# Optimization experiments

Measured on AMD Instinct MI355X. Metric: run time of the kernel, lower is better.

Reference implementation:

```python
import jax, jax.numpy as jnp
import numpy as np

ATOM_VOC = 128
APO = 128
NHEAD = 16
D_MODEL = 512
BOND_VOC = 32
CHIRAL_VOC = 4
B, L = 4, 384


def setup_inputs() -> dict:
    key = jax.random.key(0)
    ks = jax.random.split(key, 12)
    atoms = jax.random.randint(ks[0], (B, L), 0, ATOM_VOC)
    chirals = jax.random.randint(ks[1], (B, L), 0, CHIRAL_VOC)
    coordinates = jax.random.normal(ks[2], (B, L, 3), dtype=jnp.float32)
    bonds = jax.random.randint(ks[3], (B, L, L), 0, BOND_VOC)
    # embedding tables; padding_idx rows (0) zeroed to match torch padding_idx
    atype_emb = jax.random.normal(ks[4], (ATOM_VOC, D_MODEL), dtype=jnp.float32) * 0.02
    atype_emb = atype_emb.at[0].set(0.0)
    chiral_emb = jax.random.normal(ks[5], (CHIRAL_VOC, D_MODEL), dtype=jnp.float32) * 0.02
    chiral_emb = chiral_emb.at[0].set(0.0)
    apair_w_emb = jax.random.normal(ks[6], (ATOM_VOC * ATOM_VOC, APO), dtype=jnp.float32) * 0.02
    apair_b_emb = jax.random.normal(ks[7], (ATOM_VOC * ATOM_VOC, APO), dtype=jnp.float32) * 0.02
    means = jax.random.normal(ks[8], (APO,), dtype=jnp.float32) * 0.1
    stds = jnp.ones((APO,), dtype=jnp.float32) + jax.random.normal(ks[9], (APO,), dtype=jnp.float32) * 0.1
    bond_emb = jax.random.normal(ks[10], (BOND_VOC, NHEAD), dtype=jnp.float32) * 0.02
    bond_emb = bond_emb.at[0].set(0.0)
    lin_w = jax.random.normal(ks[11], (NHEAD, APO), dtype=jnp.float32) * (1.0 / np.sqrt(APO))
    lin_b = jnp.zeros((NHEAD,), dtype=jnp.float32)
    return dict(atoms=atoms, chirals=chirals, coordinates=coordinates, bonds=bonds,
                atype_emb=atype_emb, chiral_emb=chiral_emb,
                apair_w_emb=apair_w_emb, apair_b_emb=apair_b_emb,
                means=means, stds=stds, bond_emb=bond_emb, lin_w=lin_w, lin_b=lin_b)


def reference(atoms, chirals, coordinates, bonds, atype_emb, chiral_emb,
              apair_w_emb, apair_b_emb, means, stds, bond_emb, lin_w, lin_b):
    # atoms: [b,l] int; coordinates: [b,l,3]; bonds: [b,l,l] int
    atoms_emb = atype_emb[atoms] + chiral_emb[chirals]          # [b,l,d]
    atoms_emb = jnp.transpose(atoms_emb, (1, 0, 2))             # [l,b,d]
    diff = coordinates[:, None, :, :] - coordinates[:, :, None, :]  # [b,l,l,3]
    d2 = jnp.sum(diff * diff, axis=-1)
    distances = jnp.sqrt(d2 + 1e-12)                            # [b,l,l] (eps avoids nan grad on diag)
    apair_idx = atoms[:, None, :] * ATOM_VOC + atoms[:, :, None]  # [b,l,l]
    ap = apair_w_emb[apair_idx] * distances[..., None] + apair_b_emb[apair_idx]  # [b,l,l,apo]
    s = jnp.abs(stds) + 1e-5
    ap = jnp.exp(-0.5 * jnp.square((ap - means) / s)) / (np.sqrt(2 * np.pi) * s)
    ap = jnp.einsum('bijk,hk->bijh', ap, lin_w) + lin_b + bond_emb[bonds]  # [b,l,l,nhead]
    pad = (atoms == 0)[:, None, :, None]                        # mask key atoms (dim 2)
    ap = jnp.where(pad, -jnp.inf, ap)
    ap = jnp.transpose(ap, (0, 3, 1, 2))                        # [b,nhead,l,l]
    return atoms_emb, ap
```

## Files before the change

kernel.cpp:

```cpp
#include <hip/hip_runtime.h>
#include <hip/hip_fp16.h>
#include <math.h>
#include <string.h>

#define ATOM_VOC 128
#define APO      128
#define NHEAD    16
#define D_MODEL  512
#define NB       4
#define NL       384

typedef __attribute__((ext_vector_type(8))) _Float16 f16x8;
typedef __attribute__((ext_vector_type(4))) float    f32x4;
typedef __attribute__((ext_vector_type(4))) unsigned u32x4;

#define PACK_DWORDS (ATOM_VOC * ATOM_VOC * APO)
#define BFT_SHORTS  (4 * 4 * 16 * 8)

static __device__ inline unsigned short f2h(float x) {
    __half h = __float2half(x);
    unsigned short u; memcpy(&u, &h, 2); return u;
}

__global__ __launch_bounds__(128) void pack_kernel(
    const float* __restrict__ apw, const float* __restrict__ apb,
    const float* __restrict__ means, const float* __restrict__ stds,
    const float* __restrict__ lin_w,
    unsigned* __restrict__ pack, unsigned short* __restrict__ bft, int write_bft)
{
    const int t    = threadIdx.x;
    const int v    = blockIdx.x;
    const int ai   = blockIdx.y;
    const int half = t >> 6;
    const int p    = t & 63;
    const int k0   = 2 * p, k1 = 2 * p + 1;

    const float s0  = fabsf(stds[k0]) + 1e-5f;
    const float s1  = fabsf(stds[k1]) + 1e-5f;
    const float ag0 = 0.84932180028802f / s0;
    const float ag1 = 0.84932180028802f / s1;

    const size_t srcrow = ((size_t)v * ATOM_VOC + ai) * APO;
    float x0, x1;
    if (half == 0) {
        x0 = apw[srcrow + k0] * ag0;
        x1 = apw[srcrow + k1] * ag1;
    } else {
        x0 = (apb[srcrow + k0] - means[k0]) * ag0;
        x1 = (apb[srcrow + k1] - means[k1]) * ag1;
    }
    pack[((size_t)ai * ATOM_VOC + v) * APO + half * 64 + p] =
        ((unsigned)f2h(x1) << 16) | f2h(x0);

    if (write_bft && v == 0 && ai == 0) {
#pragma unroll
        for (int hh = 0; hh < 2; ++hh) {
            const int cid  = t + hh * 128;
            const int ks   = cid >> 6;
            const int quad = (cid >> 4) & 3;
            const int h    = cid & 15;
            const int kb   = ks * 32 + quad * 8;
            unsigned short tmp[8];
#pragma unroll
            for (int u = 0; u < 8; ++u) {
                const int kk = kb + u;
                float z = 0.3989422804014327f / (fabsf(stds[kk]) + 1e-5f);
                tmp[u] = f2h(lin_w[h * APO + kk] * z);
            }
            memcpy(&bft[(size_t)cid * 8], tmp, 16);
        }
    }
}

__global__ __launch_bounds__(256) void atoms_emb_kernel(
    const int* __restrict__ atoms, const int* __restrict__ chirals,
    const float* __restrict__ atype_emb, const float* __restrict__ chiral_emb,
    float* __restrict__ out)
{
    const int D4 = D_MODEL / 4;
    int t = blockIdx.x * 256 + threadIdx.x;
    if (t >= NL * NB * D4) return;
    int d4 = t % D4;
    int bl = t / D4;
    int b  = bl % NB;
    int l  = bl / NB;
    int a  = atoms[b * NL + l];
    int c  = chirals[b * NL + l];
    float4 va = ((const float4*)(atype_emb  + (size_t)a * D_MODEL))[d4];
    float4 vc = ((const float4*)(chiral_emb + (size_t)c * D_MODEL))[d4];
    float4 o;
    o.x = va.x + vc.x; o.y = va.y + vc.y; o.z = va.z + vc.z; o.w = va.w + vc.w;
    ((float4*)out)[t] = o;
}

__global__ __launch_bounds__(512, 4) void ap_kernel(
    const int*            __restrict__ atoms,
    const float*          __restrict__ coords,
    const int*            __restrict__ bonds,
    const unsigned*       __restrict__ pack,
    const unsigned short* __restrict__ bft,
    const float*          __restrict__ bond_emb,
    const float*          __restrict__ lin_b,
    float*                __restrict__ out)
{
    const int i    = blockIdx.x;
    const int b    = blockIdx.y;
    const int t    = threadIdx.x;
    const int lane = t & 63;
    const int wave = t >> 6;
    const int h    = lane & 15;
    const int quad = lane >> 4;

    __shared__ unsigned tbl[ATOM_VOC * APO];

    const int ai = atoms[b * NL + i];

    const unsigned* src = pack + (size_t)ai * (ATOM_VOC * APO);
#pragma unroll
    for (int it = 0; it < 8; ++it) {
        int c    = it * 512 + t;
        int v    = c >> 5;
        int cc   = c & 31;
        int hlf  = cc >> 4;
        int cp   = cc & 15;
        u32x4 d  = ((const u32x4*)src)[c];
        *(u32x4*)&tbl[v * APO + hlf * 64 + 4 * (cp ^ (v & 15))] = d;
    }

    f16x8 bfrag[4];
#pragma unroll
    for (int ks = 0; ks < 4; ++ks)
        memcpy(&bfrag[ks], bft + ((size_t)((ks * 4 + quad) * 16 + h)) * 8, 16);
    const float lbh = lin_b[h];

    const float cix = coords[((size_t)b * NL + i) * 3 + 0];
    const float ciy = coords[((size_t)b * NL + i) * 3 + 1];
    const float ciz = coords[((size_t)b * NL + i) * 3 + 2];

    int     jv[3];
    __half2 jd2[3];
#pragma unroll
    for (int it = 0; it < 3; ++it) {
        const int j = it * 128 + wave * 16 + h;
        jv[it] = atoms[b * NL + j];
        const float dx = coords[((size_t)b * NL + j) * 3 + 0] - cix;
        const float dy = coords[((size_t)b * NL + j) * 3 + 1] - ciy;
        const float dz = coords[((size_t)b * NL + j) * 3 + 2] - ciz;
        jd2[it] = __half2half2(__float2half(
            sqrtf(fmaf(dx, dx, fmaf(dy, dy, dz * dz)) + 1e-12f)));
    }

    __syncthreads();

    const size_t bondrow = ((size_t)b * NL + i) * NL;
    float* op = out + (((size_t)(b * NHEAD + h)) * NL + i) * NL;

    u32x4 pa[2][8];
    int   bidx[2][4], aje[2][4];

#define ISSUE(itc, s)                                                         \
    {                                                                         \
        const int v_    = jv[itc];                                            \
        const int vb_   = v_ * APO;                                           \
        const int vx_   = v_ & 15;                                            \
        _Pragma("unroll")                                                     \
        for (int cc = 0; cc < 8; ++cc) {                                      \
            const int ks_ = cc >> 1, e_ = cc & 1;                             \
            pa[s][cc] = *(const u32x4*)&tbl[vb_ + e_ * 64 +                   \
                                           4 * ((ks_ * 4 + quad) ^ vx_)];     \
        }                                                                     \
        const int jb_ = itc * 128 + wave * 16 + quad * 4;                     \
        _Pragma("unroll")                                                     \
        for (int r = 0; r < 4; ++r) {                                         \
            bidx[s][r] = bonds[bondrow + jb_ + r];                            \
            aje[s][r]  = atoms[b * NL + jb_ + r];                             \
        }                                                                     \
    }

    ISSUE(0, 0)

#pragma unroll
    for (int it = 0; it < 3; ++it) {
        const int s = it & 1;
        if (it < 2) ISSUE(it + 1, (it + 1) & 1)

        const __half2 d2 = jd2[it];
        f32x4 acc = {0.f, 0.f, 0.f, 0.f};
#pragma unroll
        for (int ks = 0; ks < 4; ++ks) {
            const u32x4 wch = pa[s][ks * 2 + 0];
            const u32x4 bch = pa[s][ks * 2 + 1];
            unsigned afw[4];
#pragma unroll
            for (int q = 0; q < 4; ++q) {
                __half2 w2, b2;
                unsigned wd = wch[q], bd = bch[q];
                memcpy(&w2, &wd, 4); memcpy(&b2, &bd, 4);
                __half2 u2  = __hfma2(w2, d2, b2);
                __half2 nm2 = __hmul2(u2, __hneg2(u2));
                __half2 g2  = h2exp2(nm2);
                memcpy(&afw[q], &g2, 4);
            }
            f16x8 af;
            memcpy(&af, afw, 16);
            acc = __builtin_amdgcn_mfma_f32_16x16x32_f16(af, bfrag[ks], acc, 0, 0, 0);
        }

        const int jb = it * 128 + wave * 16 + quad * 4;
#pragma unroll
        for (int r = 0; r < 4; ++r) {
            float vv = acc[r] + lbh + bond_emb[bidx[s][r] * NHEAD + h];
            if (aje[s][r] == 0) vv = -1.0e30f;
            op[jb + r] = vv;
        }
    }
#undef ISSUE
}

extern "C" void kernel_launch(void* const* d_in, const int* in_sizes, int n_in,
                              void* d_out, int out_size, void* d_ws, size_t ws_size,
                              hipStream_t stream)
{
    const int*   atoms      = (const int*)d_in[0];
    const int*   chirals    = (const int*)d_in[1];
    const float* coords     = (const float*)d_in[2];
    const int*   bonds      = (const int*)d_in[3];
    const float* atype_emb  = (const float*)d_in[4];
    const float* chiral_emb = (const float*)d_in[5];
    const float* apw        = (const float*)d_in[6];
    const float* apb        = (const float*)d_in[7];
    const float* means      = (const float*)d_in[8];
    const float* stds       = (const float*)d_in[9];
    const float* bond_emb   = (const float*)d_in[10];
    const float* lin_w      = (const float*)d_in[11];
    const float* lin_b      = (const float*)d_in[12];
    float* out = (float*)d_out;

    unsigned* pack = (unsigned*)d_ws;
    unsigned short* bftp = (unsigned short*)((char*)d_ws + (size_t)PACK_DWORDS * 4);

    pack_kernel<<<dim3(ATOM_VOC, ATOM_VOC), dim3(128), 0, stream>>>(
        apw, apb, means, stds, lin_w, pack, bftp, 1);

    {
        const int total = NL * NB * (D_MODEL / 4);
        atoms_emb_kernel<<<dim3((total + 255) / 256), dim3(256), 0, stream>>>(
            atoms, chirals, atype_emb, chiral_emb, out);
    }
    {
        float* out2 = out + (size_t)NL * NB * D_MODEL;
        ap_kernel<<<dim3(NL, NB), dim3(512), 0, stream>>>(
            atoms, coords, bonds, pack, bftp, bond_emb, lin_b, out2);
    }
}
```

Baseline: 135.6 us.

## Halve LDS table by staging packed pair table in two K-phases

Packed pair-embedding layout is rearranged so each half of the K dimension is contiguous. The AP kernel now stages only half the per-atom table (32 KB instead of 64 KB LDS) per phase, with two load/sync phases, and accumulates three MFMA results across phases. Launch bounds are raised to 8 blocks per CU. The aim is higher occupancy, at the cost of an extra barrier and reloading, and the software prefetch of table rows and bond indices is dropped.

```diff
diff --git a/kernel.cpp b/kernel.cpp
--- a/kernel.cpp
+++ b/kernel.cpp
@@ -49,7 +49,8 @@
         x0 = (apb[srcrow + k0] - means[k0]) * ag0;
         x1 = (apb[srcrow + k1] - means[k1]) * ag1;
     }
-    pack[((size_t)ai * ATOM_VOC + v) * APO + half * 64 + p] =
+    const int dst = (p >> 5) * 64 + half * 32 + (p & 31);
+    pack[((size_t)ai * ATOM_VOC + v) * APO + dst] =
         ((unsigned)f2h(x1) << 16) | f2h(x0);
 
     if (write_bft && v == 0 && ai == 0) {
@@ -93,7 +94,7 @@
     ((float4*)out)[t] = o;
 }
 
-__global__ __launch_bounds__(512, 4) void ap_kernel(
+__global__ __launch_bounds__(512, 8) void ap_kernel(
     const int*            __restrict__ atoms,
     const float*          __restrict__ coords,
     const int*            __restrict__ bonds,
@@ -111,21 +112,10 @@
     const int h    = lane & 15;
     const int quad = lane >> 4;
 
-    __shared__ unsigned tbl[ATOM_VOC * APO];
+    __shared__ unsigned tbl[ATOM_VOC * 64];
 
     const int ai = atoms[b * NL + i];
-
     const unsigned* src = pack + (size_t)ai * (ATOM_VOC * APO);
-#pragma unroll
-    for (int it = 0; it < 8; ++it) {
-        int c    = it * 512 + t;
-        int v    = c >> 5;
-        int cc   = c & 31;
-        int hlf  = cc >> 4;
-        int cp   = cc & 15;
-        u32x4 d  = ((const u32x4*)src)[c];
-        *(u32x4*)&tbl[v * APO + hlf * 64 + 4 * (cp ^ (v & 15))] = d;
-    }
 
     f16x8 bfrag[4];
 #pragma unroll
@@ -150,71 +140,64 @@
             sqrtf(fmaf(dx, dx, fmaf(dy, dy, dz * dz)) + 1e-12f)));
     }
 
-    __syncthreads();
+    f32x4 acc[3] = {{0.f,0.f,0.f,0.f},{0.f,0.f,0.f,0.f},{0.f,0.f,0.f,0.f}};
+
+#pragma unroll
+    for (int ph = 0; ph < 2; ++ph) {
+        if (ph) __syncthreads();
+#pragma unroll
+        for (int itx = 0; itx < 4; ++itx) {
+            int c   = itx * 512 + t;
+            int row = c >> 4;
+            int cc  = c & 15;
+            u32x4 d = ((const u32x4*)src)[row * 32 + ph * 16 + cc];
+            *(u32x4*)&tbl[row * 64 + 4 * (cc ^ (row & 15))] = d;
+        }
+        __syncthreads();
+
+#pragma unroll
+        for (int it = 0; it < 3; ++it) {
+            const int v  = jv[it];
+            const int vb = v * 64;
+            const int vx = v & 15;
+            const __half2 d2 = jd2[it];
+#pragma unroll
+            for (int ks2 = 0; ks2 < 2; ++ks2) {
+                const u32x4 wch = *(const u32x4*)&tbl[vb + 4 * ((ks2 * 4 + quad) ^ vx)];
+                const u32x4 bch = *(const u32x4*)&tbl[vb + 4 * ((8 + ks2 * 4 + quad) ^ vx)];
+                unsigned afw[4];
+#pragma unroll
+                for (int q = 0; q < 4; ++q) {
+                    __half2 w2, b2;
+                    unsigned wd = wch[q], bd = bch[q];
+                    memcpy(&w2, &wd, 4); memcpy(&b2, &bd, 4);
+                    __half2 u2  = __hfma2(w2, d2, b2);
+                    __half2 nm2 = __hmul2(u2, __hneg2(u2));
+                    __half2 g2  = h2exp2(nm2);
+                    memcpy(&afw[q], &g2, 4);
+                }
+                f16x8 af;
+                memcpy(&af, afw, 16);
+                acc[it] = __builtin_amdgcn_mfma_f32_16x16x32_f16(
+                    af, bfrag[ph * 2 + ks2], acc[it], 0, 0, 0);
+            }
+        }
+    }
 
     const size_t bondrow = ((size_t)b * NL + i) * NL;
     float* op = out + (((size_t)(b * NHEAD + h)) * NL + i) * NL;
-
-    u32x4 pa[2][8];
-    int   bidx[2][4], aje[2][4];
-
-#define ISSUE(itc, s)                                                         \
-    {                                                                         \
-        const int v_    = jv[itc];                                            \
-        const int vb_   = v_ * APO;                                           \
-        const int vx_   = v_ & 15;                                            \
-        _Pragma("unroll")                                                     \
-        for (int cc = 0; cc < 8; ++cc) {                                      \
-            const int ks_ = cc >> 1, e_ = cc & 1;                             \
-            pa[s][cc] = *(const u32x4*)&tbl[vb_ + e_ * 64 +                   \
-                                           4 * ((ks_ * 4 + quad) ^ vx_)];     \
-        }                                                                     \
-        const int jb_ = itc * 128 + wave * 16 + quad * 4;                     \
-        _Pragma("unroll")                                                     \
-        for (int r = 0; r < 4; ++r) {                                         \
-            bidx[s][r] = bonds[bondrow + jb_ + r];                            \
-            aje[s][r]  = atoms[b * NL + jb_ + r];                             \
-        }                                                                     \
-    }
-
-    ISSUE(0, 0)
-
 #pragma unroll
     for (int it = 0; it < 3; ++it) {
-        const int s = it & 1;
-        if (it < 2) ISSUE(it + 1, (it + 1) & 1)
-
-        const __half2 d2 = jd2[it];
-        f32x4 acc = {0.f, 0.f, 0.f, 0.f};
-#pragma unroll
-        for (int ks = 0; ks < 4; ++ks) {
-            const u32x4 wch = pa[s][ks * 2 + 0];
-            const u32x4 bch = pa[s][ks * 2 + 1];
-            unsigned afw[4];
-#pragma unroll
-            for (int q = 0; q < 4; ++q) {
-                __half2 w2, b2;
-                unsigned wd = wch[q], bd = bch[q];
-                memcpy(&w2, &wd, 4); memcpy(&b2, &bd, 4);
-                __half2 u2  = __hfma2(w2, d2, b2);
-                __half2 nm2 = __hmul2(u2, __hneg2(u2));
-                __half2 g2  = h2exp2(nm2);
-                memcpy(&afw[q], &g2, 4);
-            }
-            f16x8 af;
-            memcpy(&af, afw, 16);
-            acc = __builtin_amdgcn_mfma_f32_16x16x32_f16(af, bfrag[ks], acc, 0, 0, 0);
-        }
-
         const int jb = it * 128 + wave * 16 + quad * 4;
 #pragma unroll
         for (int r = 0; r < 4; ++r) {
-            float vv = acc[r] + lbh + bond_emb[bidx[s][r] * NHEAD + h];
-            if (aje[s][r] == 0) vv = -1.0e30f;
+            const int bidx = bonds[bondrow + jb + r];
+            const int ajr  = atoms[b * NL + jb + r];
+            float vv = acc[it][r] + lbh + bond_emb[bidx * NHEAD + h];
+            if (ajr == 0) vv = -1.0e30f;
             op[jb + r] = vv;
         }
     }
-#undef ISSUE
 }
 
 extern "C" void kernel_launch(void* const* d_in, const int* in_sizes, int n_in,
```

Result: faster. 131.4 us (-3.1%).
